# Kernel optimization log

Measured on AMD Instinct MI355X. Metric: run time of the kernel, lower is better.

Reference implementation:

```python
import jax, jax.numpy as jnp
import numpy as np

NUM_NODES = 100000
HIDDEN = 128
HEADS = 8
HEAD_DIM = HIDDEN // HEADS
TDIM = 64   # Time2Vec output dim
RDIM = 64   # relation feature dim
B = 4096    # batch of target nodes
N = 64      # padded neighbor count per node
START_T = 0.2
END_T = 0.8
NORM = 1.0 / np.sqrt(HEAD_DIM)


def setup_inputs() -> dict:
    key = jax.random.key(0)
    ks = jax.random.split(key, 20)
    f = lambda k, shp: jax.random.normal(k, shp, dtype=jnp.float32)
    inp = {
        'k_tab': f(ks[0], (NUM_NODES, HIDDEN)),
        'q_tab': f(ks[1], (NUM_NODES, HIDDEN)),
        'v_tab': f(ks[2], (NUM_NODES, HIDDEN)),
        'nid': jax.random.randint(ks[3], (B,), 0, NUM_NODES),
        'neighbors': jax.random.randint(ks[4], (B, N), 0, NUM_NODES),
        'times': jax.random.uniform(ks[5], (B, N), dtype=jnp.float32),
        'rels': f(ks[6], (B, N, RDIM)),
        # Time2Vec params: first channel linear, rest sin
        't2v_w': f(ks[7], (TDIM,)) * 0.1,
        't2v_b': f(ks[8], (TDIM,)) * 0.1,
        # time_params KQV (Linear TDIM -> HIDDEN)
        'tW_k': f(ks[9], (TDIM, HIDDEN)) * 0.1, 'tb_k': f(ks[10], (HIDDEN,)) * 0.1,
        'tW_q': f(ks[11], (TDIM, HIDDEN)) * 0.1, 'tb_q': f(ks[12], (HIDDEN,)) * 0.1,
        'tW_v': f(ks[13], (TDIM, HIDDEN)) * 0.1, 'tb_v': f(ks[14], (HIDDEN,)) * 0.1,
        # edge_params KQV (only k and v branches are used by the module)
        'rW_k': f(ks[15], (RDIM, HIDDEN)) * 0.1, 'rb_k': f(ks[16], (HIDDEN,)) * 0.1,
        'rW_v': f(ks[17], (RDIM, HIDDEN)) * 0.1, 'rb_v': f(ks[18], (HIDDEN,)) * 0.1,
    }
    return inp


def _time2vec(t, w, b):
    # t: [..., 1-broadcast scalar time per entry]; returns [..., TDIM]
    f = t[..., None] * w + b
    return jnp.concatenate([f[..., :1], jnp.sin(f[..., 1:])], axis=-1)


def reference(k_tab, q_tab, v_tab, nid, neighbors, times, rels,
              t2v_w, t2v_b, tW_k, tb_k, tW_q, tb_q, tW_v, tb_v,
              rW_k, rb_k, rW_v, rb_v):
    # time-window mask (replaces data-dependent nonzero selection)
    mask = (times >= START_T) & (times < END_T)              # [B, N]
    any_valid = mask.any(axis=-1)                             # [B]

    # t2v over cat([start_t], times) as in original
    t_cat = jnp.concatenate(
        [jnp.full((times.shape[0], 1), START_T, times.dtype), times], axis=1)  # [B, N+1]
    tv = _time2vec(t_cat, t2v_w, t2v_b)                       # [B, N+1, TDIM]
    t_k = tv @ tW_k + tb_k                                    # [B, N+1, H]
    t_q = tv @ tW_q + tb_q
    t_v = tv @ tW_v + tb_v

    r_k = rels @ rW_k + rb_k                                  # [B, N, H]
    r_v = rels @ rW_v + rb_v

    q = q_tab[nid] + t_q[:, 0]                                # [B, H]
    k = k_tab[neighbors] + r_k + t_k[:, 1:]                   # [B, N, H]
    v = v_tab[neighbors] + r_v + t_v[:, 1:]                   # [B, N, H]

    Bn = q.shape[0]
    qh = q.reshape(Bn, HEADS, HEAD_DIM)
    kh = k.reshape(Bn, N, HEADS, HEAD_DIM)
    vh = v.reshape(Bn, N, HEADS, HEAD_DIM)

    scores = jnp.einsum('bhd,bnhd->bhn', qh, kh) * NORM       # [B, heads, N]
    scores = jnp.where(mask[:, None, :], scores, -1e30)
    attn = jax.nn.softmax(scores, axis=-1)
    out = jnp.einsum('bhn,bnhd->bhd', attn, vh).reshape(Bn, HIDDEN)
    # original returns zeros when no neighbors fall in the window
    return jnp.where(any_valid[:, None], out, 0.0)
```

## Files before the change

### kernel.cpp

```cpp
#include <hip/hip_runtime.h>
#include <hip/hip_bf16.h>

#define NUM_NODES 100000
#define BATCH 4096
#define NNB 64
#define HID 128
#define NHEAD 8
#define HDIM 16
#define TDIM 64
#define RDIM 64
#define START_TC 0.2f
#define END_TC 0.8f
#define NORMS 0.25f

typedef __attribute__((ext_vector_type(4))) float f32x4;
typedef __attribute__((ext_vector_type(2))) float f32x2;
typedef __attribute__((ext_vector_type(8))) short bf16x8;

#define AST 136
#define KST 130
#define APAD 10

__device__ __forceinline__ short fb(float f) {
    __hip_bfloat16 h = __float2bfloat16(f);
    return *reinterpret_cast<short*>(&h);
}

__global__ void prep_kernel(const float* __restrict__ t2v_w, const float* __restrict__ t2v_b,
                            const float* __restrict__ tW_k, const float* __restrict__ tb_k,
                            const float* __restrict__ tW_q, const float* __restrict__ tb_q,
                            const float* __restrict__ tW_v, const float* __restrict__ tb_v,
                            const float* __restrict__ rW_k, const float* __restrict__ rb_k,
                            const float* __restrict__ rW_v, const float* __restrict__ rb_v,
                            short* __restrict__ wfrag, float* __restrict__ bias_kv,
                            float* __restrict__ q0_add)
{
    int blk = blockIdx.x, t = threadIdx.x;
    if (blk < 128) {
        int idx = blk * 256 + t;
        int i   = idx & 7;
        int ln  = (idx >> 3) & 63;
        int nt  = (idx >> 9) & 15;
        int kt  = idx >> 13;
        int k = kt * 32 + (ln >> 4) * 8 + i;
        int c = nt * 16 + (ln & 15);
        int cc = (c < HID) ? c : c - HID;
        float val;
        if (k < TDIM) val = (c < HID) ? tW_k[k*HID + cc] : tW_v[k*HID + cc];
        else          val = (c < HID) ? rW_k[(k-TDIM)*HID + cc] : rW_v[(k-TDIM)*HID + cc];
        wfrag[idx] = fb(val);
    } else if (blk == 128) {
        bias_kv[t] = (t < HID) ? (tb_k[t] + rb_k[t]) : (tb_v[t-HID] + rb_v[t-HID]);
    } else if (t < HID) {
        float s = tb_q[t];
        for (int j = 0; j < TDIM; ++j) {
            float f = START_TC * t2v_w[j] + t2v_b[j];
            float tv = (j == 0) ? f : __sinf(f);
            s += tv * tW_q[j*HID + t];
        }
        q0_add[t] = s;
    }
}

__launch_bounds__(512, 6)
__global__ void aggr_kernel(const float* __restrict__ k_tab, const float* __restrict__ q_tab,
                            const float* __restrict__ v_tab,
                            const int* __restrict__ nid, const int* __restrict__ neighbors,
                            const float* __restrict__ times, const float* __restrict__ rels,
                            const float* __restrict__ t2v_w, const float* __restrict__ t2v_b,
                            const short* __restrict__ wfrag, const float* __restrict__ bias_kv,
                            const float* __restrict__ q0_add, float* __restrict__ out)
{
    __shared__ __align__(16) short AK[64 * AST];
    __shared__ __align__(16) float q_lds[HID];
    __shared__ float maskadd[NNB];
    __shared__ int   nb_lds[NNB];
    __shared__ __align__(16) float attn_t[NNB][APAD];
    __shared__ int   anyvalid;

    short* A   = AK;
    short* Ksh = AK;

    const int b = blockIdx.x;
    const int t = threadIdx.x;
    const int w = t >> 6;
    const int l = t & 63;

    const bf16x8* wf = (const bf16x8*)wfrag;
    bf16x8 bfr[4][2];
    #pragma unroll
    for (int kt = 0; kt < 4; ++kt)
        #pragma unroll
        for (int j = 0; j < 2; ++j)
            bfr[kt][j] = wf[(kt*16 + (2*w + j))*64 + l];

    if (t < 64) {
        float tt = times[b*NNB + t];
        bool valid = (tt >= START_TC) && (tt < END_TC);
        nb_lds[t] = valid ? neighbors[b*NNB + t] : 0;
        maskadd[t] = valid ? 0.f : -1e30f;
        unsigned long long bal = __ballot(valid);
        if (t == 0) anyvalid = (bal != 0ull) ? 1 : 0;
    } else if (t < 96) {
        int i = t - 64;
        int q_node = nid[b];
        f32x4 qa = *(const f32x4*)(q_tab + (size_t)q_node*HID + i*4);
        f32x4 qb = *(const f32x4*)(q0_add + i*4);
        *(f32x4*)(q_lds + i*4) = qa + qb;
    }

    if (w < 4) {
        float tt = times[b*NNB + l];
        int c0 = w * 16;
        bf16x8 v0, v1;
        #pragma unroll
        for (int u = 0; u < 8; ++u) {
            int j = c0 + u;
            float f = fmaf(tt, t2v_w[j], t2v_b[j]);
            v0[u] = fb((j == 0) ? f : __sinf(f));
        }
        #pragma unroll
        for (int u = 0; u < 8; ++u) {
            int j = c0 + 8 + u;
            float f = fmaf(tt, t2v_w[j], t2v_b[j]);
            v1[u] = fb(__sinf(f));
        }
        *(bf16x8*)(&A[l*AST + c0])     = v0;
        *(bf16x8*)(&A[l*AST + c0 + 8]) = v1;
    } else {
        int s = w - 4;
        float tt = times[b*NNB + l];
        bool valid = (tt >= START_TC) && (tt < END_TC);
        int lrow = valid ? l : 0;
        const float* rp = rels + ((size_t)b*NNB + lrow)*RDIM + s*16;
        f32x4 r0 = *(const f32x4*)(rp);
        f32x4 r1 = *(const f32x4*)(rp + 4);
        f32x4 r2 = *(const f32x4*)(rp + 8);
        f32x4 r3 = *(const f32x4*)(rp + 12);
        bf16x8 o0, o1;
        #pragma unroll
        for (int e = 0; e < 4; ++e) {
            o0[e]   = fb(r0[e]);  o0[e+4] = fb(r1[e]);
            o1[e]   = fb(r2[e]);  o1[e+4] = fb(r3[e]);
        }
        *(bf16x8*)(&A[l*AST + TDIM + s*16])     = o0;
        *(bf16x8*)(&A[l*AST + TDIM + s*16 + 8]) = o1;
    }
    __syncthreads();

    f32x4 acc[4][2];
    #pragma unroll
    for (int mt = 0; mt < 4; ++mt)
        #pragma unroll
        for (int j = 0; j < 2; ++j)
            acc[mt][j] = (f32x4){0.f, 0.f, 0.f, 0.f};

    #pragma unroll
    for (int kt = 0; kt < 4; ++kt) {
        bf16x8 af[4];
        int kcol = kt*32 + (l >> 4)*8;
        #pragma unroll
        for (int mt = 0; mt < 4; ++mt)
            af[mt] = *(const bf16x8*)(&A[(mt*16 + (l & 15))*AST + kcol]);
        #pragma unroll
        for (int mt = 0; mt < 4; ++mt)
            #pragma unroll
            for (int j = 0; j < 2; ++j)
                acc[mt][j] = __builtin_amdgcn_mfma_f32_16x16x32_bf16(af[mt], bfr[kt][j], acc[mt][j], 0, 0, 0);
    }
    __syncthreads();

    if (w < 4) {
        int cw = w * 32;
        float biasr[2];
        #pragma unroll
        for (int j = 0; j < 2; ++j)
            biasr[j] = bias_kv[cw + j*16 + (l & 15)];
        #pragma unroll
        for (int mt = 0; mt < 4; ++mt) {
            float k0v[4], k1v[4];
            #pragma unroll
            for (int i = 0; i < 4; ++i) {
                int n = mt*16 + ((l >> 4) << 2) + i;
                const float* trow = k_tab + (size_t)nb_lds[n]*HID + cw + (l & 15);
                k0v[i] = trow[0];
                k1v[i] = trow[16];
            }
            #pragma unroll
            for (int i = 0; i < 4; ++i) {
                int n = mt*16 + ((l >> 4) << 2) + i;
                Ksh[n*KST + cw +      (l & 15)] = fb(acc[mt][0][i] + biasr[0] + k0v[i]);
                Ksh[n*KST + cw + 16 + (l & 15)] = fb(acc[mt][1][i] + biasr[1] + k1v[i]);
            }
        }
    } else {
        int cw = (w - 4) * 32;
        float biasr[2];
        #pragma unroll
        for (int j = 0; j < 2; ++j)
            biasr[j] = bias_kv[HID + cw + j*16 + (l & 15)];
        #pragma unroll
        for (int mt = 0; mt < 4; ++mt) {
            float v0v[4], v1v[4];
            #pragma unroll
            for (int i = 0; i < 4; ++i) {
                int n = mt*16 + ((l >> 4) << 2) + i;
                const float* trow = v_tab + (size_t)nb_lds[n]*HID + cw + (l & 15);
                v0v[i] = trow[0];
                v1v[i] = trow[16];
            }
            #pragma unroll
            for (int i = 0; i < 4; ++i) {
                acc[mt][0][i] += biasr[0] + v0v[i];
                acc[mt][1][i] += biasr[1] + v1v[i];
            }
        }
    }
    __syncthreads();

    {
        const short* krow = &Ksh[l*KST + w*16];
        float s = 0.f;
        #pragma unroll
        for (int e = 0; e < 8; ++e) {
            unsigned u = *(const unsigned*)(&krow[2*e]);
            float k0 = __uint_as_float(u << 16);
            float k1 = __uint_as_float(u & 0xffff0000u);
            s = fmaf(q_lds[w*16 + 2*e],     k0, s);
            s = fmaf(q_lds[w*16 + 2*e + 1], k1, s);
        }
        float sc = s * NORMS + maskadd[l];
        float m = sc;
        #pragma unroll
        for (int off = 1; off <= 32; off <<= 1)
            m = fmaxf(m, __shfl_xor(m, off));
        float e = __expf(sc - m);
        float sum = e;
        #pragma unroll
        for (int off = 1; off <= 32; off <<= 1)
            sum += __shfl_xor(sum, off);
        attn_t[l][w] = e / sum;
    }
    __syncthreads();

    if (w >= 4) {
        int g = w - 4;
        float p[2] = {0.f, 0.f};
        #pragma unroll
        for (int mt = 0; mt < 4; ++mt) {
            #pragma unroll
            for (int i = 0; i < 4; ++i) {
                int n = mt*16 + ((l >> 4) << 2) + i;
                f32x2 at = *(const f32x2*)(&attn_t[n][2*g]);
                p[0] = fmaf(at[0], acc[mt][0][i], p[0]);
                p[1] = fmaf(at[1], acc[mt][1][i], p[1]);
            }
        }
        #pragma unroll
        for (int j = 0; j < 2; ++j) {
            p[j] += __shfl_xor(p[j], 16);
            p[j] += __shfl_xor(p[j], 32);
        }
        if (l < 16) {
            #pragma unroll
            for (int j = 0; j < 2; ++j) {
                int col = g*32 + j*16 + l;
                out[(size_t)b*HID + col] = anyvalid ? p[j] : 0.f;
            }
        }
    }
}

extern "C" void kernel_launch(void* const* d_in, const int* in_sizes, int n_in,
                              void* d_out, int out_size, void* d_ws, size_t ws_size,
                              hipStream_t stream)
{
    const float* k_tab = (const float*)d_in[0];
    const float* q_tab = (const float*)d_in[1];
    const float* v_tab = (const float*)d_in[2];
    const int*   nid   = (const int*)d_in[3];
    const int*   neighbors = (const int*)d_in[4];
    const float* times = (const float*)d_in[5];
    const float* rels  = (const float*)d_in[6];
    const float* t2v_w = (const float*)d_in[7];
    const float* t2v_b = (const float*)d_in[8];
    const float* tW_k  = (const float*)d_in[9];
    const float* tb_k  = (const float*)d_in[10];
    const float* tW_q  = (const float*)d_in[11];
    const float* tb_q  = (const float*)d_in[12];
    const float* tW_v  = (const float*)d_in[13];
    const float* tb_v  = (const float*)d_in[14];
    const float* rW_k  = (const float*)d_in[15];
    const float* rb_k  = (const float*)d_in[16];
    const float* rW_v  = (const float*)d_in[17];
    const float* rb_v  = (const float*)d_in[18];

    short* wfrag   = (short*)d_ws;
    float* bias_kv = (float*)((char*)d_ws + 65536);
    float* q0_add  = (float*)((char*)d_ws + 65536 + 1024);

    prep_kernel<<<130, 256, 0, stream>>>(t2v_w, t2v_b, tW_k, tb_k, tW_q, tb_q,
                                         tW_v, tb_v, rW_k, rb_k, rW_v, rb_v,
                                         wfrag, bias_kv, q0_add);
    aggr_kernel<<<BATCH, 512, 0, stream>>>(k_tab, q_tab, v_tab, nid, neighbors,
                                           times, rels, t2v_w, t2v_b,
                                           wfrag, bias_kv, q0_add, (float*)d_out);
}
```

Before: 49.76 us.

## Interleave weight-fragment columns so each lane gathers adjacent column pairs

Permutes the prepacked weight fragment columns so MFMA tile j of a lane covers interleaved columns 2*d+j rather than d and d+16. Each lane can then fetch k_tab/v_tab rows as float2 vectors, write packed bf16 pairs to LDS, and store output as float2. This halves the number of gather load instructions and LDS stores in the epilogue. The attention head index per lane changes, so the weighted sum reads one attn value per row instead of two.

```diff
diff --git a/kernel.cpp b/kernel.cpp
--- a/kernel.cpp
+++ b/kernel.cpp
@@ -43,7 +43,7 @@
         int nt  = (idx >> 9) & 15;
         int kt  = idx >> 13;
         int k = kt * 32 + (ln >> 4) * 8 + i;
-        int c = nt * 16 + (ln & 15);
+        int c = (nt >> 1) * 32 + 2 * (ln & 15) + (nt & 1);
         int cc = (c < HID) ? c : c - HID;
         float val;
         if (k < TDIM) val = (c < HID) ? tW_k[k*HID + cc] : tW_v[k*HID + cc];
@@ -85,6 +85,7 @@
     const int t = threadIdx.x;
     const int w = t >> 6;
     const int l = t & 63;
+    const int d = l & 15;
 
     const bf16x8* wf = (const bf16x8*)wfrag;
     bf16x8 bfr[4][2];
@@ -161,7 +162,7 @@
         int kcol = kt*32 + (l >> 4)*8;
         #pragma unroll
         for (int mt = 0; mt < 4; ++mt)
-            af[mt] = *(const bf16x8*)(&A[(mt*16 + (l & 15))*AST + kcol]);
+            af[mt] = *(const bf16x8*)(&A[(mt*16 + d)*AST + kcol]);
         #pragma unroll
         for (int mt = 0; mt < 4; ++mt)
             #pragma unroll
@@ -172,47 +173,38 @@
 
     if (w < 4) {
         int cw = w * 32;
-        float biasr[2];
-        #pragma unroll
-        for (int j = 0; j < 2; ++j)
-            biasr[j] = bias_kv[cw + j*16 + (l & 15)];
+        f32x2 biasr = *(const f32x2*)(bias_kv + cw + 2*d);
         #pragma unroll
         for (int mt = 0; mt < 4; ++mt) {
-            float k0v[4], k1v[4];
-            #pragma unroll
-            for (int i = 0; i < 4; ++i) {
-                int n = mt*16 + ((l >> 4) << 2) + i;
-                const float* trow = k_tab + (size_t)nb_lds[n]*HID + cw + (l & 15);
-                k0v[i] = trow[0];
-                k1v[i] = trow[16];
-            }
-            #pragma unroll
-            for (int i = 0; i < 4; ++i) {
-                int n = mt*16 + ((l >> 4) << 2) + i;
-                Ksh[n*KST + cw +      (l & 15)] = fb(acc[mt][0][i] + biasr[0] + k0v[i]);
-                Ksh[n*KST + cw + 16 + (l & 15)] = fb(acc[mt][1][i] + biasr[1] + k1v[i]);
+            f32x2 kv[4];
+            #pragma unroll
+            for (int i = 0; i < 4; ++i) {
+                int n = mt*16 + ((l >> 4) << 2) + i;
+                kv[i] = *(const f32x2*)(k_tab + (size_t)nb_lds[n]*HID + cw + 2*d);
+            }
+            #pragma unroll
+            for (int i = 0; i < 4; ++i) {
+                int n = mt*16 + ((l >> 4) << 2) + i;
+                unsigned p0 = (unsigned)(unsigned short)fb(acc[mt][0][i] + biasr[0] + kv[i][0]);
+                unsigned p1 = (unsigned)(unsigned short)fb(acc[mt][1][i] + biasr[1] + kv[i][1]);
+                *(unsigned*)(&Ksh[n*KST + cw + 2*d]) = p0 | (p1 << 16);
             }
         }
     } else {
         int cw = (w - 4) * 32;
-        float biasr[2];
-        #pragma unroll
-        for (int j = 0; j < 2; ++j)
-            biasr[j] = bias_kv[HID + cw + j*16 + (l & 15)];
+        f32x2 biasr = *(const f32x2*)(bias_kv + HID + cw + 2*d);
         #pragma unroll
         for (int mt = 0; mt < 4; ++mt) {
-            float v0v[4], v1v[4];
-            #pragma unroll
-            for (int i = 0; i < 4; ++i) {
-                int n = mt*16 + ((l >> 4) << 2) + i;
-                const float* trow = v_tab + (size_t)nb_lds[n]*HID + cw + (l & 15);
-                v0v[i] = trow[0];
-                v1v[i] = trow[16];
-            }
-            #pragma unroll
-            for (int i = 0; i < 4; ++i) {
-                acc[mt][0][i] += biasr[0] + v0v[i];
-                acc[mt][1][i] += biasr[1] + v1v[i];
+            f32x2 vv[4];
+            #pragma unroll
+            for (int i = 0; i < 4; ++i) {
+                int n = mt*16 + ((l >> 4) << 2) + i;
+                vv[i] = *(const f32x2*)(v_tab + (size_t)nb_lds[n]*HID + cw + 2*d);
+            }
+            #pragma unroll
+            for (int i = 0; i < 4; ++i) {
+                acc[mt][0][i] += biasr[0] + vv[i][0];
+                acc[mt][1][i] += biasr[1] + vv[i][1];
             }
         }
     }
@@ -244,29 +236,26 @@
     __syncthreads();
 
     if (w >= 4) {
-        int g = w - 4;
-        float p[2] = {0.f, 0.f};
+        int gq = w - 4;
+        int hoff = 2*gq + ((d >= 8) ? 1 : 0);
+        float p0 = 0.f, p1 = 0.f;
         #pragma unroll
         for (int mt = 0; mt < 4; ++mt) {
             #pragma unroll
             for (int i = 0; i < 4; ++i) {
                 int n = mt*16 + ((l >> 4) << 2) + i;
-                f32x2 at = *(const f32x2*)(&attn_t[n][2*g]);
-                p[0] = fmaf(at[0], acc[mt][0][i], p[0]);
-                p[1] = fmaf(at[1], acc[mt][1][i], p[1]);
-            }
-        }
-        #pragma unroll
-        for (int j = 0; j < 2; ++j) {
-            p[j] += __shfl_xor(p[j], 16);
-            p[j] += __shfl_xor(p[j], 32);
-        }
+                float at = attn_t[n][hoff];
+                p0 = fmaf(at, acc[mt][0][i], p0);
+                p1 = fmaf(at, acc[mt][1][i], p1);
+            }
+        }
+        p0 += __shfl_xor(p0, 16);  p0 += __shfl_xor(p0, 32);
+        p1 += __shfl_xor(p1, 16);  p1 += __shfl_xor(p1, 32);
         if (l < 16) {
-            #pragma unroll
-            for (int j = 0; j < 2; ++j) {
-                int col = g*32 + j*16 + l;
-                out[(size_t)b*HID + col] = anyvalid ? p[j] : 0.f;
-            }
+            f32x2 st;
+            st[0] = anyvalid ? p0 : 0.f;
+            st[1] = anyvalid ? p1 : 0.f;
+            *(f32x2*)(out + (size_t)b*HID + gq*32 + 2*l) = st;
         }
     }
 }
```

After: 52.92 us. +6.3%, slower.
